# Performance work log

Hardware: AMD Instinct MI355X
Metric: run time of the kernel (lower is better)

Reference implementation:

```python
import jax, jax.numpy as jnp
import numpy as np

B, T, D, H, DK, DV, R, DFF, K = 4, 1024, 1024, 8, 128, 128, 64, 4096, 4
DECAY, THR, SBETA, EPS = 0.9, 0.5, 10.0, 1e-6


def setup_inputs() -> dict:
    key = jax.random.key(0)
    ks = jax.random.split(key, 16)
    def w(i, shape, s=0.02):
        return jax.random.normal(ks[i], shape, jnp.float32) * s
    z = lambda *shape: jnp.zeros(shape, jnp.float32)
    return {
        'x': jax.random.normal(ks[0], (B, T, D), jnp.float32),
        'state_tensor': z(B, H, DK, DV),
        'spike_mem': z(B, H, DK),
        'norm_in_w': jnp.ones((D,), jnp.float32),
        'conv_w': w(1, (D, K), 0.2),
        'conv_b': z(D),
        'q_w': w(2, (H * DK, D)),
        'k_w': w(3, (H * DK, D)),
        'v_w': w(4, (H * DV, D)),
        'out_w': w(5, (D, H * DV)),
        'spike_w': w(6, (H * DK, D), 0.5),
        'alpha_up_w': w(7, (R, D)),
        'alpha_up_b': z(R),
        'alpha_down_w': w(8, (H * DK, R)),
        'alpha_down_b': z(H * DK),
        'alpha_spike': z(1, H, DK),
        'beta_w': w(9, (H, D)),
        'beta_b': z(H),
        'beta_spike': z(1, H, DK),
        'head_norm_w': jnp.ones((H, DV), jnp.float32),
        'u1_w': w(10, (R, D)),
        'u1_b': z(R),
        'u2_w': w(11, (D, R)),
        'u2_b': z(D),
        'ff_norm_w': jnp.ones((D,), jnp.float32),
        'ff_w1': w(12, (DFF, D)),
        'ff_w3': w(13, (DFF, D)),
        'ff_w2': w(14, (D, DFF)),
    }


def _rms(x, w):
    return x * w / jnp.sqrt(jnp.mean(x * x, axis=-1, keepdims=True) + EPS)


def _forward(x, state_tensor, spike_mem, norm_in_w, conv_w, conv_b, q_w, k_w, v_w,
             out_w, spike_w, alpha_up_w, alpha_up_b, alpha_down_w, alpha_down_b,
             alpha_spike, beta_w, beta_b, beta_spike, head_norm_w, u1_w, u1_b,
             u2_w, u2_b, ff_norm_w, ff_w1, ff_w3, ff_w2):
    Bs, Ts, Ds = x.shape
    h = _rms(x, norm_in_w)
    # causal depthwise short conv, kernel K, left-padded
    hp = jnp.pad(h, ((0, 0), (K - 1, 0), (0, 0)))
    conv = conv_b + sum(hp[:, j:j + Ts, :] * conv_w[:, j] for j in range(K))
    h = jax.nn.silu(conv)
    q = (h @ q_w.T).reshape(Bs, Ts, H, DK)
    k = (h @ k_w.T).reshape(Bs, Ts, H, DK)
    v = (h @ v_w.T).reshape(Bs, Ts, H, DV)
    q = q / (jnp.linalg.norm(q, axis=-1, keepdims=True) + 1e-6)
    k = k / (jnp.linalg.norm(k, axis=-1, keepdims=True) + 1e-6)
    drive = (h @ spike_w.T).reshape(Bs, Ts, H, DK)
    a_base = (jax.nn.silu(h @ alpha_up_w.T + alpha_up_b) @ alpha_down_w.T
              + alpha_down_b).reshape(Bs, Ts, H, DK)
    b_base = h @ beta_w.T + beta_b  # [B,T,H]

    a_sp = alpha_spike[0]  # [H,DK]
    b_sp = beta_spike[0]   # [H,DK]

    def step(carry, xs):
        s, mem = carry
        qt, kt, vt, dt, at, bt = xs
        # LIF: leaky integrate, hard spike fwd + sigmoid surrogate bwd, soft reset
        mem = DECAY * mem + dt
        sp_soft = jax.nn.sigmoid(SBETA * (mem - THR))
        sp_hard = (mem > THR).astype(mem.dtype)
        spike = sp_soft + jax.lax.stop_gradient(sp_hard - sp_soft)
        mem = mem - spike * THR
        alpha = jax.nn.sigmoid(at + a_sp * spike)                          # [B,H,DK]
        beta = jax.nn.sigmoid(bt[..., None]
                              + jnp.sum(spike * b_sp, -1, keepdims=True))  # [B,H,1]
        active = jax.lax.stop_gradient(
            (jnp.sum(jnp.abs(spike), -1, keepdims=True) > 0).astype(mem.dtype))
        # gated delta-rule fast-weight update on state [B,H,DK,DV]
        s = s * alpha[..., None]
        pred = jnp.einsum('bhk,bhkv->bhv', kt, s)
        s = s + (beta * active)[..., None] * kt[..., None] * (vt - pred)[:, :, None, :]
        out = jnp.einsum('bhk,bhkv->bhv', qt, s)
        return (s, mem), out

    tm = lambda a: jnp.swapaxes(a, 0, 1)  # time-major for scan
    (_, _), ys = jax.lax.scan(
        step, (state_tensor, spike_mem),
        (tm(q), tm(k), tm(v), tm(drive), tm(a_base), tm(b_base)))
    y = jnp.swapaxes(ys, 0, 1)             # [B,T,H,DV]
    y = _rms(y, head_norm_w)               # headwise RMSNorm, weight [H,DV]
    y = y.reshape(Bs, Ts, H * DV) @ out_w.T
    gate = jax.nn.sigmoid(jax.nn.silu(x @ u1_w.T + u1_b) @ u2_w.T + u2_b)
    y = x + y * gate
    z = _rms(y, ff_norm_w)
    y = y + (jax.nn.silu(z @ ff_w1.T) * (z @ ff_w3.T)) @ ff_w2.T
    return y


def reference(x, state_tensor, spike_mem, norm_in_w, conv_w, conv_b, q_w, k_w, v_w,
              out_w, spike_w, alpha_up_w, alpha_up_b, alpha_down_w, alpha_down_b,
              alpha_spike, beta_w, beta_b, beta_spike, head_norm_w, u1_w, u1_b,
              u2_w, u2_b, ff_norm_w, ff_w1, ff_w3, ff_w2):
    return _forward(x, state_tensor, spike_mem, norm_in_w, conv_w, conv_b, q_w,
                    k_w, v_w, out_w, spike_w, alpha_up_w, alpha_up_b,
                    alpha_down_w, alpha_down_b, alpha_spike, beta_w, beta_b,
                    beta_spike, head_norm_w, u1_w, u1_b, u2_w, u2_b, ff_norm_w,
                    ff_w1, ff_w3, ff_w2)
```

## Files before the change

### kernel.cpp

```cpp
#include <hip/hip_runtime.h>
#include <hip/hip_bf16.h>
#include <stdint.h>

#define DEV static __device__ __forceinline__

typedef float f32x4 __attribute__((ext_vector_type(4)));
typedef short bf16x8 __attribute__((ext_vector_type(8)));
typedef float accf4 __attribute__((ext_vector_type(4)));
typedef unsigned short u16;
typedef unsigned int u32;
typedef unsigned long long u64;
typedef u16 u16x4 __attribute__((ext_vector_type(4)));

#define BB 4
#define TT 1024
#define DD 1024
#define HH 8
#define DKK 128
#define DVV 128
#define MM (BB*TT)
#define DFF 4096
#define SKQ 4096

DEV u16 f2b(float f){
  union { float f; u32 u; } v; v.f = f;
  u32 r = (v.u + 0x7fffu + ((v.u >> 16) & 1u)) >> 16;
  return (u16)r;
}
DEV float b2f(u16 h){
  union { u32 u; float f; } v; v.u = ((u32)h) << 16;
  return v.f;
}
DEV float sigm(float x){ return 1.f / (1.f + __expf(-x)); }
DEV float silu_f(float x){ return x / (1.f + __expf(-x)); }

DEV void gl_lds16(const void* g, void* l){
  __builtin_amdgcn_global_load_lds(
      (const __attribute__((address_space(1))) void*)g,
      (__attribute__((address_space(3))) void*)l, 16, 0, 0);
}

template<int CTRL>
DEV float dpp_add(float x){
  union { float f; int i; } u; u.f = x;
  int y = __builtin_amdgcn_update_dpp(0, u.i, CTRL, 0xf, 0xf, true);
  union { int i; float f; } w; w.i = y;
  return x + w.f;
}
DEV float red16(float x){
  x = dpp_add<0xB1>(x);
  x = dpp_add<0x4E>(x);
  x = dpp_add<0x141>(x);
  x = dpp_add<0x140>(x);
  return x;
}
DEV float red64_last(float x){
  x = red16(x);
  x = dpp_add<0x142>(x);
  x = dpp_add<0x143>(x);
  return x;
}

template<int OP>
__global__ __launch_bounds__(256) void gemm_bt(
    const u16* __restrict__ A, const u16* __restrict__ Bm,
    float* __restrict__ C, u16* __restrict__ Cb,
    const float* __restrict__ bias,
    const u64* __restrict__ spkp, const float* __restrict__ aspkp,
    int N, int K, int lda, int ldb, int ldc)
{
  __shared__ u16 lsA[2][128*64];
  __shared__ u16 lsB[2][128*64];
  const int tid = threadIdx.x;
  const int bm = blockIdx.x, bn = blockIdx.y;
  const int wid = tid >> 6, lane = tid & 63;
  const int wr = wid >> 1, wc = wid & 1;
  const int fr = lane & 15, fq = lane >> 4;
  accf4 acc[4][4];
#pragma unroll
  for (int i=0;i<4;i++)
#pragma unroll
    for (int j=0;j<4;j++) acc[i][j] = (accf4)0.f;

  const int srow = tid >> 3;
  const int sk = (tid & 7) * 8;
  const u16* aP = A + (size_t)(bm*128 + srow) * lda + sk;
  const u16* bP = Bm + (size_t)(bn*128 + srow) * ldb + sk;

  auto STAGE = [&](int buf, int t){
    char* lA = (char*)lsA[buf] + tid*16;
    char* lB = (char*)lsB[buf] + tid*16;
    const u16* a = aP + (size_t)t*64;
    const u16* b = bP + (size_t)t*64;
#pragma unroll
    for (int it=0; it<4; ++it) {
      gl_lds16(a + (size_t)it*32*lda, lA + it*4096);
      gl_lds16(b + (size_t)it*32*ldb, lB + it*4096);
    }
  };

  const int nk = K >> 6;
  STAGE(0, 0);
  asm volatile("s_waitcnt vmcnt(0)" ::: "memory");
  __syncthreads();
  int cur = 0;
  for (int t = 0; t < nk; ++t) {
    if (t + 1 < nk) STAGE(cur ^ 1, t + 1);
    const u16* la = lsA[cur];
    const u16* lb = lsB[cur];
#pragma unroll
    for (int ks=0; ks<2; ++ks) {
      bf16x8 av[4], bv[4];
#pragma unroll
      for (int i=0;i<4;i++)
        av[i] = *(const bf16x8*)&la[(wr*64 + i*16 + fr)*64 + ks*32 + fq*8];
#pragma unroll
      for (int j=0;j<4;j++)
        bv[j] = *(const bf16x8*)&lb[(wc*64 + j*16 + fr)*64 + ks*32 + fq*8];
#pragma unroll
      for (int i=0;i<4;i++)
#pragma unroll
        for (int j=0;j<4;j++)
          acc[i][j] = __builtin_amdgcn_mfma_f32_16x16x32_bf16(av[i], bv[j], acc[i][j], 0, 0, 0);
    }
    asm volatile("s_waitcnt vmcnt(0)" ::: "memory");
    __syncthreads();
    cur ^= 1;
  }

  if constexpr (OP == 3) {
#pragma unroll
    for (int i=0;i<4;i++) {
      const int r0 = bm*128 + wr*64 + i*16 + fq*4;
#pragma unroll
      for (int j=0;j<4;j+=2) {
        const int oc = bn*64 + wc*32 + (j>>1)*16 + fr;
#pragma unroll
        for (int rr=0; rr<4; ++rr) {
          Cb[(size_t)(r0+rr)*ldc + oc] =
              f2b(silu_f(acc[i][j][rr]) * acc[i][j+1][rr]);
        }
      }
    }
  } else if constexpr (OP == 4) {
#pragma unroll
    for (int i=0;i<4;i++) {
      const int r0 = bm*128 + wr*64 + i*16 + fq*4;
#pragma unroll
      for (int j=0;j<4;j++) {
        const int c = bn*128 + wc*64 + j*16 + fr;
        const int hq = c >> 7, dkh = c & 127;
        const float asv = aspkp[c];
        const float bv = bias[c];
#pragma unroll
        for (int rr=0; rr<4; ++rr) {
          const int r = r0 + rr;
          const int bq = r >> 10, tq = r & 1023;
          const u64 mask = spkp[(((size_t)(bq*8 + hq))*TT + tq)*2 + (dkh>>6)];
          const float add = ((mask >> (dkh & 63)) & 1ull) ? asv : 0.f;
          C[(size_t)r*ldc + c] = sigm(acc[i][j][rr] + bv + add);
        }
      }
    }
  } else {
#pragma unroll
    for (int i=0;i<4;i++) {
      const int r0 = bm*128 + wr*64 + i*16 + fq*4;
#pragma unroll
      for (int j=0;j<4;j++) {
        const int c = bn*128 + wc*64 + j*16 + fr;
#pragma unroll
        for (int rr=0; rr<4; ++rr) {
          const size_t idx = (size_t)(r0+rr)*ldc + c;
          float v = acc[i][j][rr];
          if (OP == 0) { if (bias) v += bias[c]; C[idx] = v; }
          if (OP == 1) { C[idx] += v; }
          if (OP == 2) { v += bias[c]; Cb[idx] = f2b(silu_f(v)); }
        }
      }
    }
  }
}

template<int OP>
__global__ __launch_bounds__(512) void gemm256(
    const u16* __restrict__ A, const u16* __restrict__ Bm,
    float* __restrict__ C, u16* __restrict__ Cb,
    int K, int lda, int ldb, int ldc)
{
  __shared__ u16 lsA[2][256*64];
  __shared__ u16 lsB[2][256*64];
  const int tid = threadIdx.x;
  const int bm = blockIdx.x, bn = blockIdx.y;
  const int wid = tid >> 6, lane = tid & 63;
  const int wr = wid >> 2, wc = wid & 3;
  const int fr = lane & 15, fq = lane >> 4;
  accf4 acc[8][4];
#pragma unroll
  for (int i=0;i<8;i++)
#pragma unroll
    for (int j=0;j<4;j++) acc[i][j] = (accf4)0.f;

  const int srow = tid >> 3;
  const int sk = (tid & 7) * 8;
  const u16* aP = A + (size_t)(bm*256 + srow) * lda + sk;
  const u16* bP = Bm + (size_t)(bn*256 + srow) * ldb + sk;

  auto STAGE = [&](int buf, int t){
    char* lA = (char*)lsA[buf] + tid*16;
    char* lB = (char*)lsB[buf] + tid*16;
    const u16* a = aP + (size_t)t*64;
    const u16* b = bP + (size_t)t*64;
#pragma unroll
    for (int it=0; it<4; ++it) {
      gl_lds16(a + (size_t)it*64*lda, lA + it*8192);
      gl_lds16(b + (size_t)it*64*ldb, lB + it*8192);
    }
  };

  const int nk = K >> 6;
  STAGE(0, 0);
  asm volatile("s_waitcnt vmcnt(0)" ::: "memory");
  __syncthreads();
  int cur = 0;
  for (int t = 0; t < nk; ++t) {
    if (t + 1 < nk) STAGE(cur ^ 1, t + 1);
    const u16* la = lsA[cur];
    const u16* lb = lsB[cur];
#pragma unroll
    for (int ks=0; ks<2; ++ks) {
      bf16x8 av[8], bv[4];
#pragma unroll
      for (int i=0;i<8;i++)
        av[i] = *(const bf16x8*)&la[(wr*128 + i*16 + fr)*64 + ks*32 + fq*8];
#pragma unroll
      for (int j=0;j<4;j++)
        bv[j] = *(const bf16x8*)&lb[(wc*64 + j*16 + fr)*64 + ks*32 + fq*8];
#pragma unroll
      for (int i=0;i<8;i++)
#pragma unroll
        for (int j=0;j<4;j++)
          acc[i][j] = __builtin_amdgcn_mfma_f32_16x16x32_bf16(av[i], bv[j], acc[i][j], 0, 0, 0);
    }
    asm volatile("s_waitcnt vmcnt(0)" ::: "memory");
    __syncthreads();
    cur ^= 1;
  }

  if constexpr (OP == 3) {
#pragma unroll
    for (int i=0;i<8;i++) {
      const int r0 = bm*256 + wr*128 + i*16 + fq*4;
#pragma unroll
      for (int j=0;j<4;j+=2) {
        const int rb = bn*256 + wc*64 + j*16 + fr;
        const int oc = (rb>>7)*64 + (((rb>>4)&7)>>1)*16 + (rb&15);
#pragma unroll
        for (int rr=0; rr<4; ++rr) {
          Cb[(size_t)(r0+rr)*ldc + oc] =
              f2b(silu_f(acc[i][j][rr]) * acc[i][j+1][rr]);
        }
      }
    }
  } else {
#pragma unroll
    for (int i=0;i<8;i++) {
      const int r0 = bm*256 + wr*128 + i*16 + fq*4;
#pragma unroll
      for (int j=0;j<4;j++) {
        const int c = bn*256 + wc*64 + j*16 + fr;
#pragma unroll
        for (int rr=0; rr<4; ++rr)
          C[(size_t)(r0+rr)*ldc + c] = acc[i][j][rr];
      }
    }
  }
}

__global__ __launch_bounds__(256) void prep_all(
    const float* __restrict__ qw, const float* __restrict__ kw,
    const float* __restrict__ vw, const float* __restrict__ sw,
    const float* __restrict__ ow, const float* __restrict__ fw1,
    const float* __restrict__ fw3, const float* __restrict__ fw2,
    const float* __restrict__ x, const float* __restrict__ aupw,
    const float* __restrict__ adnw, const float* __restrict__ betw,
    const float* __restrict__ u1w, const float* __restrict__ u2w,
    const float* __restrict__ aupb, const float* __restrict__ betb,
    const float* __restrict__ u1b,
    u16* __restrict__ wcat4, u16* __restrict__ swcat, u16* __restrict__ owb,
    u16* __restrict__ fwcat, u16* __restrict__ fw2b, u16* __restrict__ xbf,
    u16* __restrict__ aupwb, u16* __restrict__ adnwb, u16* __restrict__ betwb,
    u16* __restrict__ u1wb, u16* __restrict__ u2wb,
    float* __restrict__ aupbp, float* __restrict__ betbp, float* __restrict__ u1bp)
{
  const int bid = blockIdx.x, tid = threadIdx.x;
  auto cvt4 = [&](const float* s, u16* d, int base){
    size_t i = ((size_t)(bid - base)*256 + tid)*4;
    f32x4 v = *(const f32x4*)(s + i);
    u16x4 o; o.x=f2b(v.x); o.y=f2b(v.y); o.z=f2b(v.z); o.w=f2b(v.w);
    *(u16x4*)(d + i) = o;
  };
  auto pad4 = [&](const float* s, u16* d, int base, int sr, int sc, int dc){
    size_t i = ((size_t)(bid - base)*256 + tid)*4;
    int r = (int)(i / dc), c = (int)(i % dc);
    u16x4 o;
#pragma unroll
    for (int e=0;e<4;e++){
      float v = (r < sr && c+e < sc) ? s[(size_t)r*sc + c + e] : 0.f;
      o[e] = f2b(v);
    }
    *(u16x4*)(d + i) = o;
  };
  if (bid < 1024)       cvt4(qw, wcat4, 0);
  else if (bid < 2048)  cvt4(kw, wcat4 + (size_t)1024*1024, 1024);
  else if (bid < 3072)  cvt4(vw, wcat4 + (size_t)2*1024*1024, 2048);
  else if (bid < 4096) {
    size_t i = ((size_t)(bid - 3072)*256 + tid)*4;
    int r = (int)(i >> 10), c = (int)(i & 1023);
    f32x4 v = *(const f32x4*)(sw + i);
    u16x4 h, l;
    h.x=f2b(v.x); h.y=f2b(v.y); h.z=f2b(v.z); h.w=f2b(v.w);
    l.x=f2b(v.x-b2f(h.x)); l.y=f2b(v.y-b2f(h.y)); l.z=f2b(v.z-b2f(h.z)); l.w=f2b(v.w-b2f(h.w));
    *(u16x4*)(wcat4 + (size_t)3*1024*1024 + i) = h;
    *(u16x4*)(swcat + (size_t)r*2048 + 1024 + c) = h;
    *(u16x4*)(swcat + (size_t)r*2048 + c) = l;
  }
  else if (bid < 5120)  cvt4(ow, owb, 4096);
  else if (bid < 13312) {
    int r = bid - 5120;
    int t128 = r >> 7, s8 = (r >> 4) & 7, row16 = r & 15;
    int srow = t128*64 + (s8 >> 1)*16 + row16;
    const float* src = (s8 & 1) ? fw3 : fw1;
    size_t si = (size_t)srow*1024 + tid*4;
    f32x4 v = *(const f32x4*)(src + si);
    u16x4 o; o.x=f2b(v.x); o.y=f2b(v.y); o.z=f2b(v.z); o.w=f2b(v.w);
    *(u16x4*)(fwcat + (size_t)r*1024 + tid*4) = o;
  }
  else if (bid < 17408) cvt4(fw2, fw2b, 13312);
  else if (bid < 21504) cvt4(x, xbf, 17408);
  else if (bid < 21632) pad4(aupw, aupwb, 21504, 64, 1024, 1024);
  else if (bid < 21760) pad4(adnw, adnwb, 21632, 1024, 64, 128);
  else if (bid < 21888) pad4(betw, betwb, 21760, 8, 1024, 1024);
  else if (bid < 22016) pad4(u1w, u1wb, 21888, 64, 1024, 1024);
  else if (bid < 22144) pad4(u2w, u2wb, 22016, 1024, 64, 128);
  else if (tid < 128) {
    aupbp[tid] = tid < 64 ? aupb[tid] : 0.f;
    betbp[tid] = tid < 8  ? betb[tid] : 0.f;
    u1bp[tid]  = tid < 64 ? u1b[tid]  : 0.f;
  }
}

__global__ __launch_bounds__(256) void row_rms(const float* __restrict__ x, float* __restrict__ invr){
  int m = blockIdx.x, tid = threadIdx.x;
  f32x4 v = *(const f32x4*)(x + (size_t)m*DD + tid*4);
  float s = v.x*v.x + v.y*v.y + v.z*v.z + v.w*v.w;
#pragma unroll
  for (int msk=1; msk<64; msk<<=1) s += __shfl_xor(s, msk);
  __shared__ float ws[4];
  if ((tid&63)==0) ws[tid>>6] = s;
  __syncthreads();
  if (tid==0) invr[m] = 1.f / sqrtf((ws[0]+ws[1]+ws[2]+ws[3])*(1.f/DD) + 1e-6f);
}

__global__ __launch_bounds__(256) void conv_silu_k(
    const float* __restrict__ x, const float* __restrict__ invr,
    const float* __restrict__ nw, const float* __restrict__ cw, const float* __restrict__ cb,
    u16* __restrict__ hcat)
{
  int m = blockIdx.x, tid = threadIdx.x;
  int b = m >> 10, t = m & 1023;
  int d4 = tid * 4;
  f32x4 acc = *(const f32x4*)(cb + d4);
  f32x4 nwv = *(const f32x4*)(nw + d4);
  f32x4 w0 = *(const f32x4*)(cw + (size_t)(d4+0)*4);
  f32x4 w1 = *(const f32x4*)(cw + (size_t)(d4+1)*4);
  f32x4 w2 = *(const f32x4*)(cw + (size_t)(d4+2)*4);
  f32x4 w3 = *(const f32x4*)(cw + (size_t)(d4+3)*4);
#pragma unroll
  for (int j=0;j<4;j++) {
    int tt = t - 3 + j;
    if (tt >= 0) {
      int m2 = (b<<10) + tt;
      f32x4 xv = *(const f32x4*)(x + (size_t)m2*DD + d4);
      float sc = invr[m2];
      acc.x += xv.x * sc * nwv.x * w0[j];
      acc.y += xv.y * sc * nwv.y * w1[j];
      acc.z += xv.z * sc * nwv.z * w2[j];
      acc.w += xv.w * sc * nwv.w * w3[j];
    }
  }
  float h0 = silu_f(acc.x), h1 = silu_f(acc.y), h2 = silu_f(acc.z), h3 = silu_f(acc.w);
  size_t o = (size_t)m*2048 + d4;
  u16x4 hv; hv.x=f2b(h0); hv.y=f2b(h1); hv.z=f2b(h2); hv.w=f2b(h3);
  u16x4 lv; lv.x=f2b(h0-b2f(hv.x)); lv.y=f2b(h1-b2f(hv.y)); lv.z=f2b(h2-b2f(hv.z)); lv.w=f2b(h3-b2f(hv.w));
  *(u16x4*)(hcat + o) = hv;
  *(u16x4*)(hcat + o + 1024) = lv;
}

__global__ __launch_bounds__(256) void qk_norm(float* __restrict__ qkv){
  int gw = blockIdx.x*4 + (threadIdx.x>>6);
  int lane = threadIdx.x & 63;
  size_t off = (size_t)(gw>>3)*SKQ + (size_t)(gw&7)*DKK;
  float* q = qkv + off;
  float* k = qkv + off + 1024;
  float q1 = q[lane], q2 = q[lane+64];
  float k1 = k[lane], k2 = k[lane+64];
  float sq = q1*q1+q2*q2, sk = k1*k1+k2*k2;
#pragma unroll
  for (int msk=1; msk<64; msk<<=1){ sq += __shfl_xor(sq,msk); sk += __shfl_xor(sk,msk); }
  float iq = 1.f/(sqrtf(sq)+1e-6f), ik = 1.f/(sqrtf(sk)+1e-6f);
  q[lane]=q1*iq; q[lane+64]=q2*iq;
  k[lane]=k1*ik; k[lane+64]=k2*ik;
}

__global__ __launch_bounds__(256) void head_norm_k(
    const float* __restrict__ y, const float* __restrict__ w, u16* __restrict__ o)
{
  int gw = blockIdx.x*4 + (threadIdx.x>>6);
  int lane = threadIdx.x & 63;
  int h = gw & 7;
  size_t off = (size_t)(gw>>3)*DD + (size_t)h*DVV;
  float y1 = y[off+lane], y2 = y[off+lane+64];
  float s = y1*y1 + y2*y2;
#pragma unroll
  for (int msk=1; msk<64; msk<<=1) s += __shfl_xor(s,msk);
  float inv = 1.f / sqrtf(s*(1.f/DVV) + 1e-6f);
  o[off+lane]    = f2b(y1*inv*w[h*DVV+lane]);
  o[off+lane+64] = f2b(y2*inv*w[h*DVV+lane+64]);
}

__global__ __launch_bounds__(64) void spike_scan(
    const float* __restrict__ dr, const float* __restrict__ bbase,
    const float* __restrict__ bspk, const float* __restrict__ mem0,
    u64* __restrict__ spk, float* __restrict__ bs)
{
  __shared__ float bufA[64*128];
  __shared__ float bufB[64*128];
  __shared__ float bb_lds[TT];
  const int bh = blockIdx.x, b = bh>>3, h = bh&7;
  const int lane = threadIdx.x;

  for (int i=0;i<16;++i)
    bb_lds[i*64 + lane] = bbase[((size_t)b*TT + i*64 + lane)*128 + h];

  float m1 = mem0[bh*DKK + lane], m2 = mem0[bh*DKK + lane + 64];
  const float b1s = bspk[h*DKK+lane], b2s = bspk[h*DKK+lane+64];

  const char* drBase = (const char*)(dr + ((size_t)b*TT)*SKQ + (size_t)h*DKK);
  const int rowp = lane>>5, col = lane&31;
  asm volatile("s_waitcnt vmcnt(0) lgkmcnt(0)" ::: "memory");

  auto DMA = [&](int c){
    char* l = (char*)((c&1) ? bufB : bufA);
    const char* g = drBase + ((size_t)(c*64 + rowp)*SKQ + (size_t)col*4)*4;
#pragma unroll
    for (int j=0;j<32;++j)
      gl_lds16(g + (size_t)j*2*SKQ*4, l + j*1024);
  };

  auto CHUNK = [&](int c){
    const float* lf = (c&1) ? bufB : bufA;
    u32 q0=0,q1=0,q2=0,q3=0; float qss=0.f;
#pragma unroll 8
    for (int t=0;t<64;++t){
      float d1 = lf[t*128 + lane];
      float d2 = lf[t*128 + 64 + lane];
      m1 = 0.9f*m1 + d1; m2 = 0.9f*m2 + d2;
      bool p1 = m1 > 0.5f, p2 = m2 > 0.5f;
      u64 bl1 = __ballot(p1), bl2 = __ballot(p2);
      float sp1 = p1 ? 1.f : 0.f, sp2 = p2 ? 1.f : 0.f;
      m1 -= sp1*0.5f; m2 -= sp2*0.5f;
      float ss = red64_last(sp1*b1s + sp2*b2s);
      float ssv = __shfl(ss, 63);
      if (lane == t){
        q0=(u32)bl1; q1=(u32)(bl1>>32);
        q2=(u32)bl2; q3=(u32)(bl2>>32);
        qss=ssv;
      }
    }
    const int tg = c*64 + lane;
    float bv = bb_lds[tg];
    bool act = (q0|q1|q2|q3) != 0u;
    float beta = act ? sigm(bv + qss) : 0.f;
    u32* sp32 = (u32*)(spk + ((size_t)bh*TT + tg)*2);
    uint4 m4; m4.x=q0; m4.y=q1; m4.z=q2; m4.w=q3;
    *(uint4*)sp32 = m4;
    bs[((size_t)b*TT + tg)*HH + h] = beta;
  };

  DMA(0); DMA(1);
  for (int c=0; c<16; ++c){
    if (c == 0)       asm volatile("s_waitcnt vmcnt(32)" ::: "memory");
    else if (c < 15)  asm volatile("s_waitcnt vmcnt(34)" ::: "memory");
    else              asm volatile("s_waitcnt vmcnt(2)"  ::: "memory");
    CHUNK(c);
    if (c+2 < 16) DMA(c+2);
  }
}

__global__ __launch_bounds__(256, 1) void scan_k(
    const float* __restrict__ qkv, const float* __restrict__ al,
    const float* __restrict__ bs, const float* __restrict__ s0p,
    float* __restrict__ y)
{
  const int bx = blockIdx.x;
  const int bh = bx & 31, dvb = bx >> 5;
  const int b = bh >> 3, h = bh & 7;
  const int tid = threadIdx.x;
  const int dvl = tid >> 4, dkl = tid & 15;
  const int dv = dvb*16 + dvl;
  const int dk0 = dkl*8;

  float s[8];
  {
    const float* sp = s0p + ((size_t)bh*DKK + dk0) * DVV + dv;
#pragma unroll
    for (int i=0;i<8;i++) s[i] = sp[(size_t)i*DVV];
  }
  const size_t rq = ((size_t)b*TT)*SKQ + (size_t)h*DKK;
  const size_t ra = ((size_t)b*TT)*DD + (size_t)h*DKK;
  const float* qP = qkv + rq + dk0;
  const float* kP = qkv + rq + 1024 + dk0;
  const float* vP = qkv + rq + 2048 + dv;
  const float* aP = al + ra + dk0;
  const float* bP = bs + (size_t)b*TT*HH + h;
  float* yP = y + ra + dv;

  struct Buf { f32x4 kk[2], qq[2], aa[2]; float vv, bb; };
  Buf B0,B1,B2,B3,B4,B5,B6,B7;
  auto LOAD = [&](int t_, Buf& Bx){
    size_t o = (size_t)t_*SKQ;
    size_t oa = (size_t)t_*DD;
    Bx.kk[0] = *(const f32x4*)(kP + o); Bx.kk[1] = *(const f32x4*)(kP + o + 4);
    Bx.qq[0] = *(const f32x4*)(qP + o); Bx.qq[1] = *(const f32x4*)(qP + o + 4);
    Bx.aa[0] = *(const f32x4*)(aP + oa); Bx.aa[1] = *(const f32x4*)(aP + oa + 4);
    Bx.vv = vP[o];
    Bx.bb = bP[(size_t)t_*HH];
  };
  auto STEP = [&](const Buf& Bx, int t_){
    float pp = 0.f, pp2 = 0.f;
#pragma unroll
    for (int i=0;i<2;i++)
#pragma unroll
      for (int e=0;e<4;e++){
        float sv = s[i*4+e] * Bx.aa[i][e];
        s[i*4+e] = sv;
        if (e < 2) pp += sv * Bx.kk[i][e]; else pp2 += sv * Bx.kk[i][e];
      }
    pp = red16(pp + pp2);
    float err = Bx.bb * (Bx.vv - pp);
    float oo = 0.f, oo2 = 0.f;
#pragma unroll
    for (int i=0;i<2;i++)
#pragma unroll
      for (int e=0;e<4;e++){
        float sv = s[i*4+e] + Bx.kk[i][e] * err;
        s[i*4+e] = sv;
        if (e < 2) oo += sv * Bx.qq[i][e]; else oo2 += sv * Bx.qq[i][e];
      }
    oo = red16(oo + oo2);
    if (dkl == 0) yP[(size_t)t_*DD] = oo;
  };

#define SBAR __builtin_amdgcn_sched_barrier(0)
  LOAD(0,B0); LOAD(1,B1); LOAD(2,B2); LOAD(3,B3);
  LOAD(4,B4); LOAD(5,B5); LOAD(6,B6);
  SBAR;
  for (int t=0; t<TT; t+=8){
    LOAD(t+ 7 < TT ? t+ 7 : TT-1, B7); SBAR; STEP(B0, t);   SBAR;
    LOAD(t+ 8 < TT ? t+ 8 : TT-1, B0); SBAR; STEP(B1, t+1); SBAR;
    LOAD(t+ 9 < TT ? t+ 9 : TT-1, B1); SBAR; STEP(B2, t+2); SBAR;
    LOAD(t+10 < TT ? t+10 : TT-1, B2); SBAR; STEP(B3, t+3); SBAR;
    LOAD(t+11 < TT ? t+11 : TT-1, B3); SBAR; STEP(B4, t+4); SBAR;
    LOAD(t+12 < TT ? t+12 : TT-1, B4); SBAR; STEP(B5, t+5); SBAR;
    LOAD(t+13 < TT ? t+13 : TT-1, B5); SBAR; STEP(B6, t+6); SBAR;
    LOAD(t+14 < TT ? t+14 : TT-1, B6); SBAR; STEP(B7, t+7); SBAR;
  }
#undef SBAR
}

__global__ __launch_bounds__(256) void gate_rms_z(
    const float* __restrict__ x, const float* __restrict__ p,
    const float* __restrict__ g, const float* __restrict__ w,
    float* __restrict__ out, u16* __restrict__ zbf)
{
  const int m = blockIdx.x, tid = threadIdx.x;
  const size_t o = (size_t)m*DD + tid*4;
  f32x4 xv = *(const f32x4*)(x+o);
  f32x4 pv = *(const f32x4*)(p+o);
  f32x4 gv = *(const f32x4*)(g+o);
  f32x4 y;
  y.x = xv.x + pv.x * sigm(gv.x);
  y.y = xv.y + pv.y * sigm(gv.y);
  y.z = xv.z + pv.z * sigm(gv.z);
  y.w = xv.w + pv.w * sigm(gv.w);
  *(f32x4*)(out+o) = y;
  float ssum = y.x*y.x + y.y*y.y + y.z*y.z + y.w*y.w;
#pragma unroll
  for (int msk=1; msk<64; msk<<=1) ssum += __shfl_xor(ssum, msk);
  __shared__ float ws[4];
  if ((tid&63)==0) ws[tid>>6] = ssum;
  __syncthreads();
  float inv = 1.f / sqrtf((ws[0]+ws[1]+ws[2]+ws[3])*(1.f/DD) + 1e-6f);
  f32x4 wv = *(const f32x4*)(w + tid*4);
  u16x4 oz;
  oz.x=f2b(y.x*inv*wv.x); oz.y=f2b(y.y*inv*wv.y);
  oz.z=f2b(y.z*inv*wv.z); oz.w=f2b(y.w*inv*wv.w);
  *(u16x4*)(zbf + o) = oz;
}

extern "C" void kernel_launch(void* const* d_in, const int* in_sizes, int n_in,
                              void* d_out, int out_size, void* d_ws, size_t ws_size,
                              hipStream_t stream)
{
  (void)in_sizes; (void)n_in; (void)out_size; (void)ws_size;
  const float* x    = (const float*)d_in[0];
  const float* st0  = (const float*)d_in[1];
  const float* mem0 = (const float*)d_in[2];
  const float* nin  = (const float*)d_in[3];
  const float* cw   = (const float*)d_in[4];
  const float* cb   = (const float*)d_in[5];
  const float* qw   = (const float*)d_in[6];
  const float* kw   = (const float*)d_in[7];
  const float* vw   = (const float*)d_in[8];
  const float* ow   = (const float*)d_in[9];
  const float* sw   = (const float*)d_in[10];
  const float* aupw = (const float*)d_in[11];
  const float* aupb = (const float*)d_in[12];
  const float* adnw = (const float*)d_in[13];
  const float* adnb = (const float*)d_in[14];
  const float* aspk = (const float*)d_in[15];
  const float* betw = (const float*)d_in[16];
  const float* betb = (const float*)d_in[17];
  const float* bspk = (const float*)d_in[18];
  const float* hnw  = (const float*)d_in[19];
  const float* u1w  = (const float*)d_in[20];
  const float* u1b  = (const float*)d_in[21];
  const float* u2w  = (const float*)d_in[22];
  const float* u2b  = (const float*)d_in[23];
  const float* ffnw = (const float*)d_in[24];
  const float* fw1  = (const float*)d_in[25];
  const float* fw3  = (const float*)d_in[26];
  const float* fw2  = (const float*)d_in[27];
  float* out = (float*)d_out;

  char* wsb = (char*)d_ws;
  size_t off = 0;
  auto alloc = [&](size_t bytes)->char*{
    off = (off + 255) & ~(size_t)255;
    char* p = wsb + off; off += bytes; return p;
  };

  u16* wcat4 = (u16*)alloc((size_t)4096*DD*2);
  u16* swcat = (u16*)alloc((size_t)DD*2048*2);
  u16* owb   = (u16*)alloc((size_t)DD*DD*2);
  u16* fwcat = (u16*)alloc((size_t)2*DFF*DD*2);
  u16* fw2b  = (u16*)alloc((size_t)DD*DFF*2);
  u16* aupwb = (u16*)alloc((size_t)128*DD*2);
  u16* adnwb = (u16*)alloc((size_t)DD*128*2);
  u16* betwb = (u16*)alloc((size_t)128*DD*2);
  u16* u1wb  = (u16*)alloc((size_t)128*DD*2);
  u16* u2wb  = (u16*)alloc((size_t)DD*128*2);
  float* aupbp = (float*)alloc(128*4);
  float* betbp = (float*)alloc(128*4);
  float* u1bp  = (float*)alloc(128*4);
  u16* xbf  = (u16*)alloc((size_t)MM*DD*2);
  float* yatt  = (float*)alloc((size_t)MM*DD*4);
  u16* yattb = (u16*)alloc((size_t)MM*DD*2);
  float* invr  = (float*)alloc((size_t)MM*4);

  size_t mark = off;
  u16* hcat = (u16*)alloc((size_t)MM*2048*2);
  float* qkvd = (float*)alloc((size_t)MM*SKQ*4);
  float* abase = (float*)alloc((size_t)MM*DD*4);
  float* bbase = (float*)alloc((size_t)MM*128*4);
  float* bscale= (float*)alloc((size_t)MM*8*4);
  u64* spk = (u64*)alloc((size_t)BB*HH*TT*2*8);
  u16* gsm  = (u16*)alloc((size_t)MM*128*2);
  off = mark;
  float* proj = (float*)alloc((size_t)MM*DD*4);
  float* gpre = (float*)alloc((size_t)MM*DD*4);
  u16* zbf  = (u16*)alloc((size_t)MM*DD*2);
  u16* g1   = (u16*)alloc((size_t)MM*128*2);
  u16* ffh  = (u16*)alloc((size_t)MM*DFF*2);

  dim3 blk(256);

  prep_all<<<dim3(22145), blk, 0, stream>>>(
      qw, kw, vw, sw, ow, fw1, fw3, fw2, x, aupw, adnw, betw, u1w, u2w,
      aupb, betb, u1b,
      wcat4, swcat, owb, fwcat, fw2b, xbf, aupwb, adnwb, betwb, u1wb, u2wb,
      aupbp, betbp, u1bp);

  row_rms<<<dim3(MM), blk, 0, stream>>>(x, invr);
  conv_silu_k<<<dim3(MM), blk, 0, stream>>>(x, invr, nin, cw, cb, hcat);

  gemm256<0><<<dim3(16,16), dim3(512), 0, stream>>>(hcat, wcat4, qkvd, nullptr,
                                                    DD, 2048, DD, SKQ);
  gemm_bt<1><<<dim3(32,8), blk, 0, stream>>>(hcat, swcat, qkvd+3072, nullptr, nullptr,
                                             nullptr, nullptr, DD, 2048, 2048, 2048, SKQ);
  gemm_bt<0><<<dim3(32,1), blk, 0, stream>>>(hcat, betwb, bbase, nullptr, betbp,
                                             nullptr, nullptr, 128, DD, 2048, DD, 128);
  spike_scan<<<dim3(BB*HH), dim3(64), 0, stream>>>(qkvd+3072, bbase, bspk, mem0, spk, bscale);
  gemm_bt<2><<<dim3(32,1), blk, 0, stream>>>(hcat, aupwb, nullptr, gsm, aupbp,
                                             nullptr, nullptr, 128, DD, 2048, DD, 128);
  gemm_bt<4><<<dim3(32,8), blk, 0, stream>>>(gsm, adnwb, abase, nullptr, adnb,
                                             spk, aspk, DD, 128, 128, 128, DD);

  qk_norm<<<dim3(MM*HH/4), blk, 0, stream>>>(qkvd);
  scan_k<<<dim3(BB*HH*8), blk, 0, stream>>>(qkvd, abase, bscale, st0, yatt);
  head_norm_k<<<dim3(MM*HH/4), blk, 0, stream>>>(yatt, hnw, yattb);

  gemm_bt<0><<<dim3(32,8), blk, 0, stream>>>(yattb, owb, proj, nullptr, nullptr,
                                             nullptr, nullptr, DD, DD, DD, DD, DD);
  gemm_bt<2><<<dim3(32,1), blk, 0, stream>>>(xbf, u1wb, nullptr, g1, u1bp,
                                             nullptr, nullptr, 128, DD, DD, DD, 128);
  gemm_bt<0><<<dim3(32,8), blk, 0, stream>>>(g1, u2wb, gpre, nullptr, u2b,
                                             nullptr, nullptr, DD, 128, 128, 128, DD);
  gate_rms_z<<<dim3(MM), blk, 0, stream>>>(x, proj, gpre, ffnw, out, zbf);

  gemm256<3><<<dim3(16,32), dim3(512), 0, stream>>>(zbf, fwcat, nullptr, ffh,
                                                    DD, DD, DD, DFF);
  gemm_bt<1><<<dim3(32,8), blk, 0, stream>>>(ffh, fw2b, out, nullptr, nullptr,
                                             nullptr, nullptr, DD, DFF, DFF, DFF, DD);
}
```

Before: 815.1 us.

## Co-schedule spike scan and scan with independent small gate GEMMs in fused launches

Turns the spike-scan, the sequential attention scan and the gemm_bt kernel into device-function bodies and launches them together in two heterogeneous 'fat' kernels. The latency-bound scans, which occupy few blocks, now share a launch with independent small GEMMs (alpha-up, u1, u2), so those GEMMs fill idle CUs and several launches go away. Shared memory is set to the largest user (about 68KB for fatA), and spike_scan now runs in 256-thread blocks with most threads idle. gpre and g1 buffers are moved out of the reused region so they stay live across the earlier phases.

New measurement: 699.3 us. -14.2%, faster.

```diff
diff --git a/kernel.cpp b/kernel.cpp
--- a/kernel.cpp
+++ b/kernel.cpp
@@ -62,17 +62,19 @@
 }
 
 template<int OP>
-__global__ __launch_bounds__(256) void gemm_bt(
+DEV void gemm128_body(
     const u16* __restrict__ A, const u16* __restrict__ Bm,
     float* __restrict__ C, u16* __restrict__ Cb,
     const float* __restrict__ bias,
     const u64* __restrict__ spkp, const float* __restrict__ aspkp,
-    int N, int K, int lda, int ldb, int ldc)
-{
-  __shared__ u16 lsA[2][128*64];
-  __shared__ u16 lsB[2][128*64];
+    int N, int K, int lda, int ldb, int ldc,
+    int bm, int bn, char* smem)
+{
+  u16* lsA0 = (u16*)smem;
+  u16* lsA1 = (u16*)(smem + 16384);
+  u16* lsB0 = (u16*)(smem + 32768);
+  u16* lsB1 = (u16*)(smem + 49152);
   const int tid = threadIdx.x;
-  const int bm = blockIdx.x, bn = blockIdx.y;
   const int wid = tid >> 6, lane = tid & 63;
   const int wr = wid >> 1, wc = wid & 1;
   const int fr = lane & 15, fq = lane >> 4;
@@ -88,8 +90,8 @@
   const u16* bP = Bm + (size_t)(bn*128 + srow) * ldb + sk;
 
   auto STAGE = [&](int buf, int t){
-    char* lA = (char*)lsA[buf] + tid*16;
-    char* lB = (char*)lsB[buf] + tid*16;
+    char* lA = (char*)(buf ? lsA1 : lsA0) + tid*16;
+    char* lB = (char*)(buf ? lsB1 : lsB0) + tid*16;
     const u16* a = aP + (size_t)t*64;
     const u16* b = bP + (size_t)t*64;
 #pragma unroll
@@ -106,8 +108,8 @@
   int cur = 0;
   for (int t = 0; t < nk; ++t) {
     if (t + 1 < nk) STAGE(cur ^ 1, t + 1);
-    const u16* la = lsA[cur];
-    const u16* lb = lsB[cur];
+    const u16* la = cur ? lsA1 : lsA0;
+    const u16* lb = cur ? lsB1 : lsB0;
 #pragma unroll
     for (int ks=0; ks<2; ++ks) {
       bf16x8 av[4], bv[4];
@@ -180,6 +182,19 @@
       }
     }
   }
+}
+
+template<int OP>
+__global__ __launch_bounds__(256) void gemm_bt(
+    const u16* __restrict__ A, const u16* __restrict__ Bm,
+    float* __restrict__ C, u16* __restrict__ Cb,
+    const float* __restrict__ bias,
+    const u64* __restrict__ spkp, const float* __restrict__ aspkp,
+    int N, int K, int lda, int ldb, int ldc)
+{
+  __shared__ __align__(16) char smem[65536];
+  gemm128_body<OP>(A, Bm, C, Cb, bias, spkp, aspkp, N, K, lda, ldb, ldc,
+                   blockIdx.x, blockIdx.y, smem);
 }
 
 template<int OP>
@@ -429,16 +444,19 @@
   o[off+lane+64] = f2b(y2*inv*w[h*DVV+lane+64]);
 }
 
-__global__ __launch_bounds__(64) void spike_scan(
+DEV void spike_body(
+    int bh, char* smem,
     const float* __restrict__ dr, const float* __restrict__ bbase,
     const float* __restrict__ bspk, const float* __restrict__ mem0,
     u64* __restrict__ spk, float* __restrict__ bs)
 {
-  __shared__ float bufA[64*128];
-  __shared__ float bufB[64*128];
-  __shared__ float bb_lds[TT];
-  const int bh = blockIdx.x, b = bh>>3, h = bh&7;
-  const int lane = threadIdx.x;
+  const int tid = threadIdx.x;
+  if (tid >= 64) return;
+  float* bufA = (float*)smem;
+  float* bufB = (float*)(smem + 32768);
+  float* bb_lds = (float*)(smem + 65536);
+  const int b = bh>>3, h = bh&7;
+  const int lane = tid;
 
   for (int i=0;i<16;++i)
     bb_lds[i*64 + lane] = bbase[((size_t)b*TT + i*64 + lane)*128 + h];
@@ -498,12 +516,12 @@
   }
 }
 
-__global__ __launch_bounds__(256, 1) void scan_k(
+DEV void scan_body(
+    int bx,
     const float* __restrict__ qkv, const float* __restrict__ al,
     const float* __restrict__ bs, const float* __restrict__ s0p,
     float* __restrict__ y)
 {
-  const int bx = blockIdx.x;
   const int bh = bx & 31, dvb = bx >> 5;
   const int b = bh >> 3, h = bh & 7;
   const int tid = threadIdx.x;
@@ -577,6 +595,46 @@
     LOAD(t+14 < TT ? t+14 : TT-1, B6); SBAR; STEP(B7, t+7); SBAR;
   }
 #undef SBAR
+}
+
+__global__ __launch_bounds__(256) void fatA(
+    const float* __restrict__ dr, const float* __restrict__ bbase,
+    const float* __restrict__ bspk, const float* __restrict__ mem0,
+    u64* __restrict__ spk, float* __restrict__ bs,
+    const u16* __restrict__ hcat, const u16* __restrict__ aupwb,
+    u16* __restrict__ gsm, const float* __restrict__ aupbp,
+    const u16* __restrict__ xbf, const u16* __restrict__ u1wb,
+    u16* __restrict__ g1, const float* __restrict__ u1bp)
+{
+  __shared__ __align__(16) char smem[69632];
+  const int bx = blockIdx.x;
+  if (bx < 32) {
+    spike_body(bx, smem, dr, bbase, bspk, mem0, spk, bs);
+  } else if (bx < 64) {
+    gemm128_body<2>(hcat, aupwb, nullptr, gsm, aupbp, nullptr, nullptr,
+                    128, DD, 2048, DD, 128, bx - 32, 0, smem);
+  } else {
+    gemm128_body<2>(xbf, u1wb, nullptr, g1, u1bp, nullptr, nullptr,
+                    128, DD, DD, DD, 128, bx - 64, 0, smem);
+  }
+}
+
+__global__ __launch_bounds__(256) void fatB(
+    const float* __restrict__ qkv, const float* __restrict__ al,
+    const float* __restrict__ bs, const float* __restrict__ s0p,
+    float* __restrict__ y,
+    const u16* __restrict__ g1, const u16* __restrict__ u2wb,
+    float* __restrict__ gpre, const float* __restrict__ u2b)
+{
+  __shared__ __align__(16) char smem[65536];
+  const int bx = blockIdx.x;
+  if (bx < 256) {
+    scan_body(bx, qkv, al, bs, s0p, y);
+  } else {
+    const int idx = bx - 256;
+    gemm128_body<0>(g1, u2wb, gpre, nullptr, u2b, nullptr, nullptr,
+                    DD, 128, 128, 128, DD, idx & 31, idx >> 5, smem);
+  }
 }
 
 __global__ __launch_bounds__(256) void gate_rms_z(
@@ -677,12 +735,13 @@
   float* bscale= (float*)alloc((size_t)MM*8*4);
   u64* spk = (u64*)alloc((size_t)BB*HH*TT*2*8);
   u16* gsm  = (u16*)alloc((size_t)MM*128*2);
-  off = mark;
+  u16* g1e  = (u16*)alloc((size_t)MM*128*2);
+  float* gpre = (float*)alloc((size_t)MM*DD*4);
+  size_t mark2 = off;
   float* proj = (float*)alloc((size_t)MM*DD*4);
-  float* gpre = (float*)alloc((size_t)MM*DD*4);
   u16* zbf  = (u16*)alloc((size_t)MM*DD*2);
-  u16* g1   = (u16*)alloc((size_t)MM*128*2);
   u16* ffh  = (u16*)alloc((size_t)MM*DFF*2);
+  (void)mark; (void)mark2;
 
   dim3 blk(256);
 
@@ -701,22 +760,19 @@
                                              nullptr, nullptr, DD, 2048, 2048, 2048, SKQ);
   gemm_bt<0><<<dim3(32,1), blk, 0, stream>>>(hcat, betwb, bbase, nullptr, betbp,
                                              nullptr, nullptr, 128, DD, 2048, DD, 128);
-  spike_scan<<<dim3(BB*HH), dim3(64), 0, stream>>>(qkvd+3072, bbase, bspk, mem0, spk, bscale);
-  gemm_bt<2><<<dim3(32,1), blk, 0, stream>>>(hcat, aupwb, nullptr, gsm, aupbp,
-                                             nullptr, nullptr, 128, DD, 2048, DD, 128);
+  fatA<<<dim3(96), blk, 0, stream>>>(qkvd+3072, bbase, bspk, mem0, spk, bscale,
+                                     hcat, aupwb, gsm, aupbp,
+                                     xbf, u1wb, g1e, u1bp);
   gemm_bt<4><<<dim3(32,8), blk, 0, stream>>>(gsm, adnwb, abase, nullptr, adnb,
                                              spk, aspk, DD, 128, 128, 128, DD);
 
   qk_norm<<<dim3(MM*HH/4), blk, 0, stream>>>(qkvd);
-  scan_k<<<dim3(BB*HH*8), blk, 0, stream>>>(qkvd, abase, bscale, st0, yatt);
+  fatB<<<dim3(512), blk, 0, stream>>>(qkvd, abase, bscale, st0, yatt,
+                                      g1e, u2wb, gpre, u2b);
   head_norm_k<<<dim3(MM*HH/4), blk, 0, stream>>>(yatt, hnw, yattb);
 
   gemm_bt<0><<<dim3(32,8), blk, 0, stream>>>(yattb, owb, proj, nullptr, nullptr,
                                              nullptr, nullptr, DD, DD, DD, DD, DD);
-  gemm_bt<2><<<dim3(32,1), blk, 0, stream>>>(xbf, u1wb, nullptr, g1, u1bp,
-                                             nullptr, nullptr, 128, DD, DD, DD, 128);
-  gemm_bt<0><<<dim3(32,8), blk, 0, stream>>>(g1, u2wb, gpre, nullptr, u2b,
-                                             nullptr, nullptr, DD, 128, 128, 128, DD);
   gate_rms_z<<<dim3(MM), blk, 0, stream>>>(x, proj, gpre, ffnw, out, zbf);
 
   gemm256<3><<<dim3(16,32), dim3(512), 0, stream>>>(zbf, fwcat, nullptr, ffh,
```
